# Performance work log

Measured on AMD Instinct MI355X. Metric: run time of the kernel, lower is better.

## Reference

```python
import jax, jax.numpy as jnp
import numpy as np

MEX_C = 2.0 / (np.sqrt(3.0) * np.pi ** 0.25)

def mexican_hat(z):
    return MEX_C * (z * z - 1.0) * jnp.exp(-0.5 * z * z)

def setup_inputs() -> dict:
    key = jax.random.key(0)
    ks = jax.random.split(key, 5)
    B, T, D, O = 4, 2048, 128, 128
    x = jax.random.normal(ks[0], (B, T, D), dtype=jnp.float32)
    # init like torch: scale ~ U(0.5,1.5), translation ~ U(-0.5,0.5), kaiming-ish weights
    scale = jax.random.uniform(ks[1], (O, D), dtype=jnp.float32, minval=0.5, maxval=1.5)
    translation = jax.random.uniform(ks[2], (O, D), dtype=jnp.float32, minval=-0.5, maxval=0.5)
    bound = 1.0 / np.sqrt(D)
    wavelet_weights = jax.random.uniform(ks[3], (O, D), dtype=jnp.float32, minval=-bound, maxval=bound)
    base_w = jax.random.uniform(ks[4], (O, D), dtype=jnp.float32, minval=-bound, maxval=bound)
    ln_gamma = jnp.ones((D,), dtype=jnp.float32)
    ln_beta = jnp.zeros((D,), dtype=jnp.float32)
    return {"x": x, "scale": scale, "translation": translation,
            "wavelet_weights": wavelet_weights, "base_w": base_w,
            "ln_gamma": ln_gamma, "ln_beta": ln_beta}

def reference(x, scale, translation, wavelet_weights, base_w, ln_gamma, ln_beta):
    B, T, D = x.shape
    O = wavelet_weights.shape[0]
    # LayerNorm over last dim (eps = 1e-5, torch default)
    mu = jnp.mean(x, axis=-1, keepdims=True)
    var = jnp.mean((x - mu) ** 2, axis=-1, keepdims=True)
    x_norm = (x - mu) / jnp.sqrt(var + 1e-5) * ln_gamma + ln_beta
    x_flat = x_norm.reshape(B * T, D)                      # (N, D)
    s = jax.nn.softplus(scale) + 0.1                       # (O, D)
    # broadcast intermediate (N, O, D) — the memory-bound path
    z = (x_flat[:, None, :] - translation[None]) / s[None]
    w = jnp.clip(mexican_hat(z), -10.0, 10.0)              # (N, O, D)
    wavelet_out = jnp.einsum('nod,od->no', w, wavelet_weights)
    base_out = x.reshape(B * T, D) @ base_w.T              # base uses raw x
    out = wavelet_out + jax.nn.silu(base_out)
    return out.reshape(B, T, O)
```

## Files before the change

kernel.cpp:

```cpp
#include <hip/hip_runtime.h>


#define D_DIM 128
#define O_DIM 128
#define ROWS  16
#define BLOCK 1024
#define CHUNK 32
#define NCHUNK (D_DIM / CHUNK)
#define XSTRIDE 9

#define C1     0.72134752f
#define SQRT_C 0.84932180f
#define WWK    1.2023651f
#define LOG2E  1.44269504f

typedef float v2f __attribute__((ext_vector_type(2)));

__device__ __forceinline__ unsigned bf16r(float f) {
    unsigned u = __float_as_uint(f);
    return (u + 0x7fffu + ((u >> 16) & 1u)) >> 16;
}

__global__ __launch_bounds__(256) void wavekan_prep(
    const float* __restrict__ scale,
    const float* __restrict__ trans,
    const float* __restrict__ ww,
    const float* __restrict__ bw,
    uint2* __restrict__ wsW)
{
    int idx = blockIdx.x * blockDim.x + threadIdx.x;
    if (idx >= O_DIM * D_DIM) return;
    int o = idx >> 7;
    int d = idx & (D_DIM - 1);
    float sc = scale[idx];
    float sp = fmaxf(sc, 0.0f) + log1pf(__expf(-fabsf(sc)));
    float is2 = SQRT_C / (sp + 0.1f);
    uint2 w;
    w.x = bf16r(trans[idx] * is2) | (bf16r(is2) << 16);
    w.y = bf16r(ww[idx] * WWK)    | (bf16r(bw[idx]) << 16);
    wsW[d * O_DIM + o] = w;
}

template<bool USE_WS>
__global__ __launch_bounds__(BLOCK, 8) void wavekan_main(
    const float* __restrict__ x,
    const float* __restrict__ scale,
    const float* __restrict__ trans,
    const float* __restrict__ ww,
    const float* __restrict__ bw,
    const float* __restrict__ gamma,
    const float* __restrict__ beta,
    const uint2* __restrict__ wsW,
    float* __restrict__ out,
    int N)
{
    __shared__ float4 s_x[D_DIM * XSTRIDE];
    __shared__ uint4  s_w4[CHUNK * O_DIM / 2];

    const int tid  = threadIdx.x;
    const int row0 = blockIdx.x * ROWS;

    {
        const int r  = tid >> 6;
        const int j  = tid & 63;
        const int d0 = j * 2;
        const int grow = row0 + r;

        float2 v2 = make_float2(0.f, 0.f);
        if (grow < N)
            v2 = *reinterpret_cast<const float2*>(x + (size_t)grow * D_DIM + d0);

        float sum = v2.x + v2.y;
        float ssq = v2.x * v2.x + v2.y * v2.y;
        #pragma unroll
        for (int m = 1; m < 64; m <<= 1) {
            sum += __shfl_xor(sum, m, 64);
            ssq += __shfl_xor(ssq, m, 64);
        }
        const float mean = sum * (1.0f / D_DIM);
        const float var  = ssq * (1.0f / D_DIM) - mean * mean;
        const float rstd = rsqrtf(var + 1e-5f);

        float2 g2 = *reinterpret_cast<const float2*>(gamma + d0);
        float2 b2 = *reinterpret_cast<const float2*>(beta + d0);

        const int p  = r >> 1;
        const int h  = r & 1;
        float* c0 = reinterpret_cast<float*>(&s_x[d0 * XSTRIDE + p]);
        float* c1 = reinterpret_cast<float*>(&s_x[(d0 + 1) * XSTRIDE + p]);
        c0[h]     = (v2.x - mean) * rstd * g2.x + b2.x;
        c0[2 + h] = v2.x;
        c1[h]     = (v2.y - mean) * rstd * g2.y + b2.y;
        c1[2 + h] = v2.y;
    }

    const int o = tid & (O_DIM - 1);
    const int g = tid >> 7;
    const uint2* __restrict__ s_w = reinterpret_cast<const uint2*>(s_w4);

    v2f accw = {0.f, 0.f};
    v2f accb = {0.f, 0.f};

    if (USE_WS) {
        const uint4* __restrict__ wsWp = reinterpret_cast<const uint4*>(wsW);
        uint4 r0 = wsWp[tid];
        uint4 r1 = wsWp[tid + BLOCK];
        for (int c = 0; c < NCHUNK; ++c) {
            __syncthreads();
            s_w4[tid]         = r0;
            s_w4[tid + BLOCK] = r1;
            if (c + 1 < NCHUNK) {
                r0 = wsWp[(c + 1) * (CHUNK * O_DIM / 2) + tid];
                r1 = wsWp[(c + 1) * (CHUNK * O_DIM / 2) + tid + BLOCK];
            }
            __syncthreads();

            #pragma unroll 8
            for (int dl = 0; dl < CHUNK; ++dl) {
                uint2 wp  = s_w[dl * O_DIM + o];
                float4 xx = s_x[(c * CHUNK + dl) * XSTRIDE + g];
                float tis = __uint_as_float(wp.x << 16);
                float isv = __uint_as_float(wp.x & 0xffff0000u);
                float wwk = __uint_as_float(wp.y << 16);
                float bwv = __uint_as_float(wp.y & 0xffff0000u);
                v2f xln = {xx.x, xx.y};
                v2f xrw = {xx.z, xx.w};
                v2f u   = xln * isv - tis;
                v2f q   = u * u;
                v2f e   = {__builtin_amdgcn_exp2f(-q.x),
                           __builtin_amdgcn_exp2f(-q.y)};
                accw += ((q - C1) * e) * wwk;
                accb += xrw * bwv;
            }
        }
    } else {
        __syncthreads();
        for (int d = 0; d < D_DIM; ++d) {
            int idx = o * D_DIM + d;
            float sc = scale[idx];
            float sp = fmaxf(sc, 0.0f) + log1pf(__expf(-fabsf(sc)));
            float is  = SQRT_C / (sp + 0.1f);
            float tws = trans[idx] * is;
            float wwk = ww[idx] * WWK;
            float bwv = bw[idx];
            float4 xx = s_x[d * XSTRIDE + g];
            v2f xln = {xx.x, xx.y};
            v2f xrw = {xx.z, xx.w};
            v2f u   = xln * is - tws;
            v2f q   = u * u;
            v2f e   = {__builtin_amdgcn_exp2f(-q.x),
                       __builtin_amdgcn_exp2f(-q.y)};
            accw += ((q - C1) * e) * wwk;
            accb += xrw * bwv;
        }
    }

    {
        const int rr0 = row0 + g * 2;
        if (rr0 < N) {
            float sig0 = 1.0f / (1.0f + __builtin_amdgcn_exp2f(-LOG2E * accb.x));
            out[(size_t)rr0 * O_DIM + o] = accw.x + accb.x * sig0;
        }
        if (rr0 + 1 < N) {
            float sig1 = 1.0f / (1.0f + __builtin_amdgcn_exp2f(-LOG2E * accb.y));
            out[(size_t)(rr0 + 1) * O_DIM + o] = accw.y + accb.y * sig1;
        }
    }
}

extern "C" void kernel_launch(void* const* d_in, const int* in_sizes, int n_in,
                              void* d_out, int out_size, void* d_ws, size_t ws_size,
                              hipStream_t stream) {
    const float* x     = (const float*)d_in[0];
    const float* scale = (const float*)d_in[1];
    const float* trans = (const float*)d_in[2];
    const float* ww    = (const float*)d_in[3];
    const float* bw    = (const float*)d_in[4];
    const float* gamma = (const float*)d_in[5];
    const float* beta  = (const float*)d_in[6];
    float* out = (float*)d_out;

    const int N = in_sizes[0] / D_DIM;
    const int grid = (N + ROWS - 1) / ROWS;

    const size_t ws_needed = (size_t)O_DIM * D_DIM * sizeof(uint2);
    if (ws_size >= ws_needed) {
        wavekan_prep<<<(O_DIM * D_DIM + 255) / 256, 256, 0, stream>>>(
            scale, trans, ww, bw, (uint2*)d_ws);
        wavekan_main<true><<<grid, BLOCK, 0, stream>>>(
            x, scale, trans, ww, bw, gamma, beta, (const uint2*)d_ws, out, N);
    } else {
        wavekan_main<false><<<grid, BLOCK, 0, stream>>>(
            x, scale, trans, ww, bw, gamma, beta, nullptr, out, N);
    }
}
```

Before: 100.6 us.

## Stream packed weights directly from global/L2 instead of staging through LDS

Removes the chunked shared-memory staging of the packed bf16 weight table and its per-chunk barriers. Each thread now loads its weight pair straight from the workspace in global memory, prefetching the next d one iteration ahead. This cuts LDS usage, which may raise occupancy, and drops the synchronisation. The cost is that every thread issues global/L2 loads per d, and the 8 row-groups in a block each re-read the same weights, relying on cache hits.

```diff
diff --git a/kernel.cpp b/kernel.cpp
--- a/kernel.cpp
+++ b/kernel.cpp
@@ -5,8 +5,6 @@
 #define O_DIM 128
 #define ROWS  16
 #define BLOCK 1024
-#define CHUNK 32
-#define NCHUNK (D_DIM / CHUNK)
 #define XSTRIDE 9
 
 #define C1     0.72134752f
@@ -55,7 +53,6 @@
     int N)
 {
     __shared__ float4 s_x[D_DIM * XSTRIDE];
-    __shared__ uint4  s_w4[CHUNK * O_DIM / 2];
 
     const int tid  = threadIdx.x;
     const int row0 = blockIdx.x * ROWS;
@@ -93,48 +90,35 @@
         c1[h]     = (v2.y - mean) * rstd * g2.y + b2.y;
         c1[2 + h] = v2.y;
     }
+    __syncthreads();
 
     const int o = tid & (O_DIM - 1);
     const int g = tid >> 7;
-    const uint2* __restrict__ s_w = reinterpret_cast<const uint2*>(s_w4);
 
     v2f accw = {0.f, 0.f};
     v2f accb = {0.f, 0.f};
 
     if (USE_WS) {
-        const uint4* __restrict__ wsWp = reinterpret_cast<const uint4*>(wsW);
-        uint4 r0 = wsWp[tid];
-        uint4 r1 = wsWp[tid + BLOCK];
-        for (int c = 0; c < NCHUNK; ++c) {
-            __syncthreads();
-            s_w4[tid]         = r0;
-            s_w4[tid + BLOCK] = r1;
-            if (c + 1 < NCHUNK) {
-                r0 = wsWp[(c + 1) * (CHUNK * O_DIM / 2) + tid];
-                r1 = wsWp[(c + 1) * (CHUNK * O_DIM / 2) + tid + BLOCK];
-            }
-            __syncthreads();
-
-            #pragma unroll 8
-            for (int dl = 0; dl < CHUNK; ++dl) {
-                uint2 wp  = s_w[dl * O_DIM + o];
-                float4 xx = s_x[(c * CHUNK + dl) * XSTRIDE + g];
-                float tis = __uint_as_float(wp.x << 16);
-                float isv = __uint_as_float(wp.x & 0xffff0000u);
-                float wwk = __uint_as_float(wp.y << 16);
-                float bwv = __uint_as_float(wp.y & 0xffff0000u);
-                v2f xln = {xx.x, xx.y};
-                v2f xrw = {xx.z, xx.w};
-                v2f u   = xln * isv - tis;
-                v2f q   = u * u;
-                v2f e   = {__builtin_amdgcn_exp2f(-q.x),
-                           __builtin_amdgcn_exp2f(-q.y)};
-                accw += ((q - C1) * e) * wwk;
-                accb += xrw * bwv;
-            }
+        uint2 w = wsW[o];
+        #pragma unroll 4
+        for (int d = 0; d < D_DIM; ++d) {
+            uint2 wn  = wsW[(((d + 1) & (D_DIM - 1)) << 7) + o];
+            float4 xx = s_x[d * XSTRIDE + g];
+            float tis = __uint_as_float(w.x << 16);
+            float isv = __uint_as_float(w.x & 0xffff0000u);
+            float wwk = __uint_as_float(w.y << 16);
+            float bwv = __uint_as_float(w.y & 0xffff0000u);
+            v2f xln = {xx.x, xx.y};
+            v2f xrw = {xx.z, xx.w};
+            v2f u   = xln * isv - tis;
+            v2f q   = u * u;
+            v2f e   = {__builtin_amdgcn_exp2f(-q.x),
+                       __builtin_amdgcn_exp2f(-q.y)};
+            accw += ((q - C1) * e) * wwk;
+            accb += xrw * bwv;
+            w = wn;
         }
     } else {
-        __syncthreads();
         for (int d = 0; d < D_DIM; ++d) {
             int idx = o * D_DIM + d;
             float sc = scale[idx];
```

Measured after the change: 100.7 us. No clear change (+0.0%).
